# Kernel tuning notes

Hardware: AMD Instinct MI355X
Metric: run time of the kernel (lower is better)

The kernel has to match this reference:

```python
import jax, jax.numpy as jnp
import numpy as np

BLANK = 0          # tf.nn.ctc_loss default blank_index (StringLookup reserves 0 for OOV)
PAD = 127          # padding_value = char_to_num.vocabulary_size()
NEG = -1e30        # log-space 'zero' (avoid -inf to keep grads NaN-free)
B, T, C, L = 1024, 256, 128, 32


def setup_inputs() -> dict:
    key = jax.random.key(0)
    k1, k2 = jax.random.split(key)
    # labels in [1, PAD-1]; none equal PAD so label_length == L (full-length labels)
    y_true = jax.random.randint(k1, (B, L), 1, PAD).astype(jnp.int32)
    y_pred = jax.random.normal(k2, (B, T, C), dtype=jnp.float32)
    return {"y_true": y_true, "y_pred": y_pred}


def _ctc_loss(y_true, y_pred):
    """Faithful jax version of tf.nn.ctc_loss(labels, logits, label_len, T,
    logits_time_major=False, blank_index=0): standard log-space alpha DP."""
    Bn, Tn, Cn = y_pred.shape
    Ln = y_true.shape[1]
    S = 2 * Ln + 1  # extended label length (blanks interleaved)

    logp = jax.nn.log_softmax(y_pred, axis=-1)                    # [B,T,C]

    # extended label sequence: blank, l1, blank, l2, ..., blank   # [B,S]
    ext = jnp.full((Bn, S), BLANK, dtype=y_true.dtype)
    ext = ext.at[:, 1::2].set(y_true)

    # log-probs gathered at extended-label symbols                # [B,T,S]
    lp_ext = jnp.take_along_axis(
        logp, jnp.broadcast_to(ext[:, None, :], (Bn, Tn, S)), axis=2)

    # label_length = count of non-padding entries (mirrors count_nonzero)
    label_len = jnp.sum(y_true != PAD, axis=1)                    # [B]

    # skip transition s-2 -> s allowed iff ext[s] is a non-blank differing
    # from ext[s-2]
    skip_ok = jnp.concatenate(
        [jnp.zeros((Bn, 2), bool),
         (ext[:, 2:] != BLANK) & (ext[:, 2:] != ext[:, :-2])], axis=1)  # [B,S]

    neg1 = jnp.full((Bn, 1), NEG, logp.dtype)
    neg2 = jnp.full((Bn, 2), NEG, logp.dtype)

    alpha0 = jnp.full((Bn, S), NEG, logp.dtype)
    alpha0 = alpha0.at[:, 0].set(lp_ext[:, 0, 0]).at[:, 1].set(lp_ext[:, 0, 1])

    def step(alpha, lp_t):  # alpha,[B,S]  lp_t,[B,S]
        a1 = jnp.concatenate([neg1, alpha[:, :-1]], axis=1)
        a2 = jnp.concatenate([neg2, alpha[:, :-2]], axis=1)
        a2 = jnp.where(skip_ok, a2, NEG)
        new = lp_t + jnp.logaddexp(jnp.logaddexp(alpha, a1), a2)
        return new, None

    lp_seq = jnp.transpose(lp_ext, (1, 0, 2))                     # [T,B,S]
    alphaT, _ = jax.lax.scan(step, alpha0, lp_seq[1:])            # [B,S]

    # total log-likelihood ends at last blank (2*len) or last label (2*len-1)
    bi = jnp.arange(Bn)
    e1 = 2 * label_len
    e2 = 2 * label_len - 1
    loglik = jnp.logaddexp(alphaT[bi, e1], alphaT[bi, e2])        # [B]
    return -loglik


def reference(y_true, y_pred):
    # The original layer returns y_pred and registers the loss via add_loss;
    # the compute-dominant quantity is the per-example CTC loss, returned here.
    return _ctc_loss(y_true, y_pred)
```

## Files before the change

kernel.cpp:

```cpp
#include <hip/hip_runtime.h>
#include <cstdint>


#define CTC_BLANK 0
#define CTC_PAD   127
#define LOG2E     1.44269504088896340736f
#define LN2       0.69314718055994530942f

constexpr int Bn = 1024, Tn = 256, Cn = 128, Ln = 32;
constexpr int NSLOT = Ln + 1;
constexpr int CR  = 8;
constexpr int NCH = Tn / CR;
constexpr int CF  = CR * Cn;

__device__ __forceinline__ float fexp2(float x) { return __builtin_amdgcn_exp2f(x); }
__device__ __forceinline__ float flog2(float x) { return __builtin_amdgcn_logf(x); }

template <int CTRL>
__device__ __forceinline__ float dpp_add(float s) {
    int v = __builtin_amdgcn_update_dpp(0, __float_as_int(s), CTRL, 0xF, 0xF, true);
    return s + __int_as_float(v);
}
__device__ __forceinline__ float dpp_wave_shr1(float src, float old) {
    return __int_as_float(__builtin_amdgcn_update_dpp(
        __float_as_int(old), __float_as_int(src), 0x138, 0xF, 0xF, false));
}
__device__ __forceinline__ void gl_lds16(const float* g, float* l) {
    __builtin_amdgcn_global_load_lds(
        (const __attribute__((address_space(1))) uint32_t*)g,
        (__attribute__((address_space(3))) uint32_t*)l, 16, 0, 0);
}

__global__ __launch_bounds__(256, 6) void ctc_fused_kernel(
        const int*   __restrict__ y_true,
        const float* __restrict__ y_pred,
        float*       __restrict__ out)
{
    __shared__ __align__(16) float raw[2][CF];
    __shared__ _Float16 Gc[Tn * NSLOT];
    __shared__ int   labels[Ln];
    __shared__ __align__(16) int cmap[Cn];
    __shared__ int   wcnt[4];
    __shared__ float partS[16];
    __shared__ float aEs[64], aOs[64];
    __shared__ int   EscS;
    int* const used = (int*)raw[1];

    const int b    = blockIdx.x;
    const int tid  = threadIdx.x;
    const int lane = tid & 63;
    const int wave = tid >> 6;
    const int half = lane >> 5;
    const int l32  = lane & 31;
    const int rotb = (b + (b >> 8)) & 3;

    const float* gbase = y_pred + (size_t)b * Tn * Cn;

    auto stage = [&](int c) {
        gl_lds16(gbase + (size_t)(c * CR + 2 * wave) * Cn + lane * 4,
                 &raw[c & 1][wave * 256]);
    };

    stage(0);

    if (tid < Ln) labels[tid] = y_true[b * Ln + tid];
    if (tid < Cn) used[tid] = 0;
    __syncthreads();
    if (tid == 0) used[CTC_BLANK] = 1;
    if (tid < Ln) used[labels[tid]] = 1;
    __syncthreads();
    {
        bool f = (tid < Cn) && (used[tid] != 0);
        unsigned long long m = __ballot(f);
        if (lane == 0) wcnt[wave] = __popcll(m);
        __syncthreads();
        int base = 0;
        for (int w = 0; w < wave; ++w) base += wcnt[w];
        if (tid < Cn)
            cmap[tid] = f ? (base + __popcll(m & ((1ull << lane) - 1ull))) : -1;
        __syncthreads();
    }

    const int4 cm = ((const int4*)cmap)[l32];
    const int rl = 2 * wave + half;
    float accE = 0.f, accO = 0.f;

    const int  i      = lane;
    const bool validO = (i < Ln);
    const bool validE = (i <= Ln);
    const int  myLab   = validO ? labels[i] : -1;
    const int  prevLab = (i >= 1 && i < Ln) ? labels[i - 1] : -1;
    const int  slotO   = validO ? cmap[myLab] : 0;
    const bool skipO   = (i >= 1 && i < Ln) &&
                         (myLab != CTC_BLANK) && (myLab != prevLab);
    const int  len = __popcll(__ballot(validO && (myLab != CTC_PAD)));
    float aE = 0.f, aO = 0.f;
    int   Esc = 0;

    auto dp_chunk = [&](int t0, int t1) {
        int t = t0;
        if (t == 0) {
            aE = (i == 0) ? fexp2((float)Gc[0])     : 0.f;
            aO = (i == 0) ? fexp2((float)Gc[slotO]) : 0.f;
            Esc = 0;
            t = 1;
        } else {
            aE  = aEs[i];
            aO  = aOs[i];
            Esc = EscS;
        }
        float pB[2], pO[2];
        const int ta = t, tb = (t + 1 < t1) ? t + 1 : t1 - 1;
        pB[0] = fexp2((float)Gc[ta * NSLOT]);
        pO[0] = fexp2((float)Gc[ta * NSLOT + slotO]);
        pB[1] = fexp2((float)Gc[tb * NSLOT]);
        pO[1] = fexp2((float)Gc[tb * NSLOT + slotO]);
        int k = 0;
        #pragma unroll 2
        for (; t < t1; ++t) {
            const float lpB = pB[k], lpO = pO[k];
            const int tp = (t + 2 < t1) ? t + 2 : t1 - 1;
            pB[k] = fexp2((float)Gc[tp * NSLOT]);
            pO[k] = fexp2((float)Gc[tp * NSLOT + slotO]);
            k ^= 1;

            const float aOup = dpp_wave_shr1(aO, 0.f);
            const float nE = lpB * (aE + aOup);
            const float nO = lpO * (aO + aE + (skipO ? aOup : 0.f));
            aE = validE ? nE : 0.f;
            aO = validO ? nO : 0.f;
        }
        float m = fmaxf(aE, aO);
        #pragma unroll
        for (int d = 1; d < 64; d <<= 1) m = fmaxf(m, __shfl_xor(m, d, 64));
        const int ex = ((__float_as_int(m) >> 23) & 255) - 127;
        const float sc = __int_as_float((127 - ex) << 23);
        aE *= sc; aO *= sc; Esc += ex;
        aEs[i] = aE;
        aOs[i] = aO;
        if (i == 0) EscS = Esc;
    };

    auto process = [&](int c, float& acc) {
        const int r = c * CR + rl;
        const float4 x = ((const float4*)&raw[c & 1][wave * 256 + half * 128])[l32];
        const float e0 = x.x * LOG2E, e1 = x.y * LOG2E,
                    e2 = x.z * LOG2E, e3 = x.w * LOG2E;
        if (cm.x >= 0) Gc[r * NSLOT + cm.x] = (_Float16)e0;
        if (cm.y >= 0) Gc[r * NSLOT + cm.y] = (_Float16)e1;
        if (cm.z >= 0) Gc[r * NSLOT + cm.z] = (_Float16)e2;
        if (cm.w >= 0) Gc[r * NSLOT + cm.w] = (_Float16)e3;
        float s = fexp2(e0) + fexp2(e1) + fexp2(e2) + fexp2(e3);
        s = dpp_add<0x111>(s);
        s = dpp_add<0x112>(s);
        s = dpp_add<0x114>(s);
        s = dpp_add<0x118>(s);
        s = dpp_add<0x142>(s);
        acc += flog2(s);
    };

    auto iter = [&](int c, float& acc) {
        if (c + 1 < NCH) stage(c + 1);
        if (c > 0 && wave == ((c - 1 + rotb) & 3))
            dp_chunk((c - 1) * CR, c * CR);
        __builtin_amdgcn_sched_barrier(0);
        if (c + 1 < NCH) asm volatile("s_waitcnt vmcnt(1)" ::: "memory");
        else             asm volatile("s_waitcnt vmcnt(0)" ::: "memory");
        __builtin_amdgcn_sched_barrier(0);
        process(c, acc);
        if (c == NCH - 1 && l32 == 31) {
            partS[rl]     = accE;
            partS[rl + 8] = accO;
        }
        asm volatile("s_waitcnt lgkmcnt(0)" ::: "memory");
        __builtin_amdgcn_s_barrier();
    };

    for (int cc = 0; cc < NCH / 2; ++cc) {
        iter(2 * cc,     accE);
        iter(2 * cc + 1, accO);
    }

    if (wave == ((NCH - 1 + rotb) & 3)) {
        dp_chunk(Tn - CR, Tn);
        const float v1 = __shfl(aE, len, 64);
        const float v2 = __shfl(aO, len - 1, 64);
        if (i == 0) {
            float S = 0.f;
            #pragma unroll
            for (int j = 0; j < 16; ++j) S += partS[j];
            const float L2 = flog2(v1 + v2) + (float)Esc;
            out[b] = LN2 * (S - L2);
        }
    }
}

extern "C" void kernel_launch(void* const* d_in, const int* in_sizes, int n_in,
                              void* d_out, int out_size, void* d_ws, size_t ws_size,
                              hipStream_t stream) {
    const int*   y_true = (const int*)d_in[0];
    const float* y_pred = (const float*)d_in[1];
    float*       out    = (float*)d_out;
    ctc_fused_kernel<<<Bn, 256, 0, stream>>>(y_true, y_pred, out);
}
```

Baseline: 195.9 us.

## Split CTC into a parallel softmax/gather kernel and a separate DP kernel

Replaces the single fused per-batch kernel with two kernels. The first runs four blocks per batch element, each computing log-sum-exp partials and gathering label-slot log-probs for 64 timesteps into a global fp16 workspace, using a 3-deep load pipeline. The second kernel is one wave per batch element that bulk-loads the gathered table into LDS and runs the full alpha recursion. The aim is to pull the serial DP off the bandwidth-bound softmax pass and raise parallelism there. The cost is an extra launch and a workspace round-trip. The old fused kernel is kept as a fallback for when no workspace is available.

Result: slower. 242.6 us (+23.8%).

```diff
diff --git a/kernel.cpp b/kernel.cpp
--- a/kernel.cpp
+++ b/kernel.cpp
@@ -9,9 +9,16 @@
 
 constexpr int Bn = 1024, Tn = 256, Cn = 128, Ln = 32;
 constexpr int NSLOT = Ln + 1;
-constexpr int CR  = 8;
-constexpr int NCH = Tn / CR;
-constexpr int CF  = CR * Cn;
+constexpr int GS    = 34;
+constexpr int ROWB  = 64;
+constexpr int CR    = 8;
+constexpr int NCHQ  = ROWB / CR;
+constexpr int GT_ROWBYTES = GS * 2;
+constexpr int GT_BBYTES   = Tn * GT_ROWBYTES;
+
+constexpr size_t WS_GT   = 0;
+constexpr size_t WS_PS   = (size_t)Bn * GT_BBYTES;
+constexpr size_t WS_NEED = WS_PS + (size_t)Bn * 64 * 4;
 
 __device__ __forceinline__ float fexp2(float x) { return __builtin_amdgcn_exp2f(x); }
 __device__ __forceinline__ float flog2(float x) { return __builtin_amdgcn_logf(x); }
@@ -31,37 +38,37 @@
         (__attribute__((address_space(3))) uint32_t*)l, 16, 0, 0);
 }
 
-__global__ __launch_bounds__(256, 6) void ctc_fused_kernel(
+__global__ __launch_bounds__(256, 8) void ctc_softmax_kernel(
         const int*   __restrict__ y_true,
         const float* __restrict__ y_pred,
-        float*       __restrict__ out)
+        _Float16*    __restrict__ Gt,
+        float*       __restrict__ psg)
 {
-    __shared__ __align__(16) float raw[2][CF];
-    __shared__ _Float16 Gc[Tn * NSLOT];
-    __shared__ int   labels[Ln];
+    __shared__ __align__(16) float raw[3][CR * Cn];
+    __shared__ __align__(16) _Float16 Gc64[ROWB * GS];
+    __shared__ int labels[Ln];
     __shared__ __align__(16) int cmap[Cn];
-    __shared__ int   wcnt[4];
-    __shared__ float partS[16];
-    __shared__ float aEs[64], aOs[64];
-    __shared__ int   EscS;
-    int* const used = (int*)raw[1];
-
-    const int b    = blockIdx.x;
+    __shared__ int used[Cn];
+    __shared__ int wcnt[4];
+
+    const int idx  = blockIdx.x;
+    const int b    = idx >> 2;
+    const int q    = idx & 3;
     const int tid  = threadIdx.x;
     const int lane = tid & 63;
     const int wave = tid >> 6;
     const int half = lane >> 5;
     const int l32  = lane & 31;
-    const int rotb = (b + (b >> 8)) & 3;
-
-    const float* gbase = y_pred + (size_t)b * Tn * Cn;
+
+    const float* gbase = y_pred + (size_t)b * Tn * Cn + (size_t)q * ROWB * Cn;
 
     auto stage = [&](int c) {
         gl_lds16(gbase + (size_t)(c * CR + 2 * wave) * Cn + lane * 4,
-                 &raw[c & 1][wave * 256]);
+                 &raw[c % 3][wave * 256]);
     };
 
     stage(0);
+    stage(1);
 
     if (tid < Ln) labels[tid] = y_true[b * Ln + tid];
     if (tid < Cn) used[tid] = 0;
@@ -85,6 +92,199 @@
     const int rl = 2 * wave + half;
     float accE = 0.f, accO = 0.f;
 
+    for (int c = 0; c < NCHQ; ++c) {
+        if (c < NCHQ - 2) stage(c + 2);
+        __builtin_amdgcn_sched_barrier(0);
+        if (c <= NCHQ - 3)      asm volatile("s_waitcnt vmcnt(2)" ::: "memory");
+        else if (c == NCHQ - 2) asm volatile("s_waitcnt vmcnt(1)" ::: "memory");
+        else                    asm volatile("s_waitcnt vmcnt(0)" ::: "memory");
+        __builtin_amdgcn_sched_barrier(0);
+
+        const int r = c * CR + rl;
+        const float4 x = ((const float4*)&raw[c % 3][wave * 256 + half * 128])[l32];
+        const float e0 = x.x * LOG2E, e1 = x.y * LOG2E,
+                    e2 = x.z * LOG2E, e3 = x.w * LOG2E;
+        if (cm.x >= 0) Gc64[r * GS + cm.x] = (_Float16)e0;
+        if (cm.y >= 0) Gc64[r * GS + cm.y] = (_Float16)e1;
+        if (cm.z >= 0) Gc64[r * GS + cm.z] = (_Float16)e2;
+        if (cm.w >= 0) Gc64[r * GS + cm.w] = (_Float16)e3;
+        float s = fexp2(e0) + fexp2(e1) + fexp2(e2) + fexp2(e3);
+        s = dpp_add<0x111>(s);
+        s = dpp_add<0x112>(s);
+        s = dpp_add<0x114>(s);
+        s = dpp_add<0x118>(s);
+        s = dpp_add<0x142>(s);
+        if (c & 1) accO += flog2(s); else accE += flog2(s);
+
+        asm volatile("s_waitcnt lgkmcnt(0)" ::: "memory");
+    }
+    if (l32 == 31) {
+        psg[b * 64 + q * 16 + rl]     = accE;
+        psg[b * 64 + q * 16 + rl + 8] = accO;
+    }
+    __syncthreads();
+
+    {
+        const uint4* src = (const uint4*)Gc64;
+        uint4* dst = (uint4*)((char*)Gt + (size_t)b * GT_BBYTES + (size_t)q * ROWB * GT_ROWBYTES);
+        dst[tid] = src[tid];
+        if (tid < 16) dst[256 + tid] = src[256 + tid];
+    }
+}
+
+__global__ __launch_bounds__(64) void ctc_dp_kernel(
+        const int*      __restrict__ y_true,
+        const _Float16* __restrict__ Gt,
+        const float*    __restrict__ psg,
+        float*          __restrict__ out)
+{
+    __shared__ __align__(16) _Float16 G[Tn * GS];
+
+    const int b = blockIdx.x;
+    const int i = threadIdx.x;
+
+    #pragma unroll
+    for (int j = 0; j < 17; ++j)
+        gl_lds16((const float*)((const char*)Gt + (size_t)b * GT_BBYTES + j * 1024) + i * 4,
+                 (float*)&G[j * 512]);
+
+    const int lr = (i < Ln) ? y_true[b * Ln + i] : CTC_PAD;
+    bool u_lo = (i == CTC_BLANK);
+    bool u_hi = false;
+    #pragma unroll
+    for (int j = 0; j < Ln; ++j) {
+        const int lj = __shfl(lr, j, 64);
+        u_lo |= (lj == i);
+        u_hi |= (lj == i + 64);
+    }
+    const unsigned long long m0 = __ballot(u_lo);
+    const unsigned long long m1 = __ballot(u_hi);
+    const int nlo = __popcll(m0);
+    auto rank = [&](int cls) -> int {
+        return (cls < 64)
+            ? __popcll(m0 & ((1ull << cls) - 1ull))
+            : nlo + __popcll(m1 & ((1ull << (cls - 64)) - 1ull));
+    };
+    const bool validO = (i < Ln);
+    const bool validE = (i <= Ln);
+    const int  myLab   = validO ? lr : -1;
+    const int  prevLab = (i >= 1 && i < Ln) ? __shfl(lr, i - 1, 64) : -1;
+    const int  slotO   = validO ? rank(lr) : 0;
+    const bool skipO   = (i >= 1 && i < Ln) &&
+                         (myLab != CTC_BLANK) && (myLab != prevLab);
+    const int  len = __popcll(__ballot(validO && (myLab != CTC_PAD)));
+
+    __builtin_amdgcn_sched_barrier(0);
+    asm volatile("s_waitcnt vmcnt(0)" ::: "memory");
+    __builtin_amdgcn_sched_barrier(0);
+
+    float aE = 0.f, aO = 0.f;
+    int   Esc = 0;
+    for (int tc = 0; tc < 32; ++tc) {
+        const int t0 = tc * 8, t1 = t0 + 8;
+        int t = t0;
+        if (t == 0) {
+            aE = (i == 0) ? fexp2((float)G[0])     : 0.f;
+            aO = (i == 0) ? fexp2((float)G[slotO]) : 0.f;
+            t = 1;
+        }
+        float pB[2], pO[2];
+        const int ta = t, tb = (t + 1 < t1) ? t + 1 : t1 - 1;
+        pB[0] = fexp2((float)G[ta * GS]);
+        pO[0] = fexp2((float)G[ta * GS + slotO]);
+        pB[1] = fexp2((float)G[tb * GS]);
+        pO[1] = fexp2((float)G[tb * GS + slotO]);
+        int k = 0;
+        #pragma unroll 2
+        for (; t < t1; ++t) {
+            const float lpB = pB[k], lpO = pO[k];
+            const int tp = (t + 2 < t1) ? t + 2 : t1 - 1;
+            pB[k] = fexp2((float)G[tp * GS]);
+            pO[k] = fexp2((float)G[tp * GS + slotO]);
+            k ^= 1;
+            const float aOup = dpp_wave_shr1(aO, 0.f);
+            const float nE = lpB * (aE + aOup);
+            const float nO = lpO * (aO + aE + (skipO ? aOup : 0.f));
+            aE = validE ? nE : 0.f;
+            aO = validO ? nO : 0.f;
+        }
+        float m = fmaxf(aE, aO);
+        #pragma unroll
+        for (int d = 1; d < 64; d <<= 1) m = fmaxf(m, __shfl_xor(m, d, 64));
+        const int ex = ((__float_as_int(m) >> 23) & 255) - 127;
+        const float sc = __int_as_float((127 - ex) << 23);
+        aE *= sc; aO *= sc; Esc += ex;
+    }
+
+    const float v1 = __shfl(aE, len, 64);
+    const float v2 = __shfl(aO, len - 1, 64);
+    if (i == 0) {
+        float S = 0.f;
+        const float4* ps = (const float4*)(psg + b * 64);
+        #pragma unroll
+        for (int j = 0; j < 16; ++j) {
+            const float4 v = ps[j];
+            S += v.x; S += v.y; S += v.z; S += v.w;
+        }
+        const float L2 = flog2(v1 + v2) + (float)Esc;
+        out[b] = LN2 * (S - L2);
+    }
+}
+
+constexpr int FNCH = Tn / CR;
+
+__global__ __launch_bounds__(256, 6) void ctc_fused_fallback(
+        const int*   __restrict__ y_true,
+        const float* __restrict__ y_pred,
+        float*       __restrict__ out)
+{
+    __shared__ __align__(16) float raw[2][CR * Cn];
+    __shared__ _Float16 Gc[Tn * NSLOT];
+    __shared__ int   labels[Ln];
+    __shared__ __align__(16) int cmap[Cn];
+    __shared__ int   wcnt[4];
+    __shared__ float partS[16];
+    __shared__ float aEs[64], aOs[64];
+    __shared__ int   EscS;
+    int* const used = (int*)raw[1];
+
+    const int b    = blockIdx.x;
+    const int tid  = threadIdx.x;
+    const int lane = tid & 63;
+    const int wave = tid >> 6;
+    const int half = lane >> 5;
+    const int l32  = lane & 31;
+    const int rotb = (b + (b >> 8)) & 3;
+
+    const float* gbase = y_pred + (size_t)b * Tn * Cn;
+    auto stage = [&](int c) {
+        gl_lds16(gbase + (size_t)(c * CR + 2 * wave) * Cn + lane * 4,
+                 &raw[c & 1][wave * 256]);
+    };
+    stage(0);
+
+    if (tid < Ln) labels[tid] = y_true[b * Ln + tid];
+    if (tid < Cn) used[tid] = 0;
+    __syncthreads();
+    if (tid == 0) used[CTC_BLANK] = 1;
+    if (tid < Ln) used[labels[tid]] = 1;
+    __syncthreads();
+    {
+        bool f = (tid < Cn) && (used[tid] != 0);
+        unsigned long long m = __ballot(f);
+        if (lane == 0) wcnt[wave] = __popcll(m);
+        __syncthreads();
+        int base = 0;
+        for (int w = 0; w < wave; ++w) base += wcnt[w];
+        if (tid < Cn)
+            cmap[tid] = f ? (base + __popcll(m & ((1ull << lane) - 1ull))) : -1;
+        __syncthreads();
+    }
+
+    const int4 cm = ((const int4*)cmap)[l32];
+    const int rl = 2 * wave + half;
+    float accE = 0.f, accO = 0.f;
+
     const int  i      = lane;
     const bool validO = (i < Ln);
     const bool validE = (i <= Ln);
@@ -105,9 +305,7 @@
             Esc = 0;
             t = 1;
         } else {
-            aE  = aEs[i];
-            aO  = aOs[i];
-            Esc = EscS;
+            aE = aEs[i]; aO = aOs[i]; Esc = EscS;
         }
         float pB[2], pO[2];
         const int ta = t, tb = (t + 1 < t1) ? t + 1 : t1 - 1;
@@ -123,7 +321,6 @@
             pB[k] = fexp2((float)Gc[tp * NSLOT]);
             pO[k] = fexp2((float)Gc[tp * NSLOT + slotO]);
             k ^= 1;
-
             const float aOup = dpp_wave_shr1(aO, 0.f);
             const float nE = lpB * (aE + aOup);
             const float nO = lpO * (aO + aE + (skipO ? aOup : 0.f));
@@ -136,8 +333,7 @@
         const int ex = ((__float_as_int(m) >> 23) & 255) - 127;
         const float sc = __int_as_float((127 - ex) << 23);
         aE *= sc; aO *= sc; Esc += ex;
-        aEs[i] = aE;
-        aOs[i] = aO;
+        aEs[i] = aE; aOs[i] = aO;
         if (i == 0) EscS = Esc;
     };
 
@@ -160,28 +356,27 @@
     };
 
     auto iter = [&](int c, float& acc) {
-        if (c + 1 < NCH) stage(c + 1);
+        if (c + 1 < FNCH) stage(c + 1);
         if (c > 0 && wave == ((c - 1 + rotb) & 3))
             dp_chunk((c - 1) * CR, c * CR);
         __builtin_amdgcn_sched_barrier(0);
-        if (c + 1 < NCH) asm volatile("s_waitcnt vmcnt(1)" ::: "memory");
-        else             asm volatile("s_waitcnt vmcnt(0)" ::: "memory");
+        if (c + 1 < FNCH) asm volatile("s_waitcnt vmcnt(1)" ::: "memory");
+        else              asm volatile("s_waitcnt vmcnt(0)" ::: "memory");
         __builtin_amdgcn_sched_barrier(0);
         process(c, acc);
-        if (c == NCH - 1 && l32 == 31) {
-            partS[rl]     = accE;
-            partS[rl + 8] = accO;
+        if (c == FNCH - 1 && l32 == 31) {
+            partS[rl] = accE; partS[rl + 8] = accO;
         }
         asm volatile("s_waitcnt lgkmcnt(0)" ::: "memory");
         __builtin_amdgcn_s_barrier();
     };
 
-    for (int cc = 0; cc < NCH / 2; ++cc) {
-        iter(2 * cc,     accE);
+    for (int cc = 0; cc < FNCH / 2; ++cc) {
+        iter(2 * cc, accE);
         iter(2 * cc + 1, accO);
     }
 
-    if (wave == ((NCH - 1 + rotb) & 3)) {
+    if (wave == ((FNCH - 1 + rotb) & 3)) {
         dp_chunk(Tn - CR, Tn);
         const float v1 = __shfl(aE, len, 64);
         const float v2 = __shfl(aO, len - 1, 64);
@@ -201,5 +396,12 @@
     const int*   y_true = (const int*)d_in[0];
     const float* y_pred = (const float*)d_in[1];
     float*       out    = (float*)d_out;
-    ctc_fused_kernel<<<Bn, 256, 0, stream>>>(y_true, y_pred, out);
-}
+    if (d_ws != nullptr && ws_size >= WS_NEED) {
+        _Float16* Gt = (_Float16*)((char*)d_ws + WS_GT);
+        float*    ps = (float*)((char*)d_ws + WS_PS);
+        ctc_softmax_kernel<<<Bn * 4, 256, 0, stream>>>(y_true, y_pred, Gt, ps);
+        ctc_dp_kernel<<<Bn, 64, 0, stream>>>(y_true, Gt, ps, out);
+    } else {
+        ctc_fused_fallback<<<Bn, 256, 0, stream>>>(y_true, y_pred, out);
+    }
+}
```
